# Optimization experiments

Hardware: AMD Instinct MI355X
Metric: run time of the kernel (lower is better)

Reference implementation:

```python
import jax, jax.numpy as jnp
import numpy as np

B, S, D, H = 2, 2048, 1024, 16
DK = D // H


def setup_inputs() -> dict:
    key = jax.random.key(0)
    ks = jax.random.split(key, 12)
    scale = 0.02
    inp = {
        "query": jax.random.normal(ks[0], (B, S, D), jnp.float32),
        "key_": jax.random.normal(ks[1], (B, S, D), jnp.float32),
        "value": jax.random.normal(ks[2], (B, S, D), jnp.float32),
        # causal mask; masked_fill where mask == 0
        "mask": jnp.tril(jnp.ones((S, S), jnp.int32))[None, None, :, :],
        # torch Linear weights are [out, in]; y = x @ W.T + b
        "Wq": jax.random.normal(ks[3], (D, D), jnp.float32) * scale,
        "bq": jax.random.normal(ks[4], (D,), jnp.float32) * scale,
        "Wk": jax.random.normal(ks[5], (D, D), jnp.float32) * scale,
        "bk": jax.random.normal(ks[6], (D,), jnp.float32) * scale,
        "Wv": jax.random.normal(ks[7], (D, D), jnp.float32) * scale,
        "bv": jax.random.normal(ks[8], (D,), jnp.float32) * scale,
        "Wo": jax.random.normal(ks[9], (D, D), jnp.float32) * scale,
        "bo": jax.random.normal(ks[10], (D,), jnp.float32) * scale,
    }
    return inp


def reference(query, key_, value, mask, Wq, bq, Wk, bk, Wv, bv, Wo, bo):
    # projections (torch Linear: x @ W.T + b)
    Q = query @ Wq.T + bq
    K = key_ @ Wk.T + bk
    V = value @ Wv.T + bv
    # [B, S, D] -> [B, H, S, DK]
    Q = Q.reshape(B, S, H, DK).transpose(0, 2, 1, 3)
    K = K.reshape(B, S, H, DK).transpose(0, 2, 1, 3)
    V = V.reshape(B, S, H, DK).transpose(0, 2, 1, 3)
    scores = jnp.einsum("bhqd,bhkd->bhqk", Q, K) / jnp.sqrt(jnp.float32(DK))
    scores = jnp.where(mask == 0, jnp.float32(-1e9), scores)
    attn = jax.nn.softmax(scores, axis=-1)
    # dropout is identity in eval mode
    context = jnp.einsum("bhqk,bhkd->bhqd", attn, V)
    context = context.transpose(0, 2, 1, 3).reshape(B, S, D)
    output = context @ Wo.T + bo
    return (output, attn)
```

## Files before the change

### kernel.cpp

```cpp
#include <hip/hip_runtime.h>
#include <hip/hip_bf16.h>

#define BB 2
#define SS 2048
#define DD 1024
#define HH 16

typedef __attribute__((ext_vector_type(8))) short bf16x8;
typedef __attribute__((ext_vector_type(4))) float f32x4;
typedef __attribute__((ext_vector_type(4))) unsigned int u32x4;
typedef __attribute__((ext_vector_type(2))) unsigned int u32x2;

__device__ inline unsigned short f2bf(float f) {
  unsigned int u = __float_as_uint(f);
  u += 0x7fff + ((u >> 16) & 1);
  return (unsigned short)(u >> 16);
}

__device__ inline void gll16(const void* g, void* l) {
  __builtin_amdgcn_global_load_lds(
      (const __attribute__((address_space(1))) unsigned int*)g,
      (__attribute__((address_space(3))) unsigned int*)l, 16, 0, 0);
}

__device__ inline int swz(int row, int col) {
  return row * 64 + ((((col >> 3) + row + (row >> 3)) & 7) << 3) + (col & 7);
}

__global__ void convert_all(const float* __restrict__ q, const float* __restrict__ k,
                            const float* __restrict__ v, const float* __restrict__ wq,
                            const float* __restrict__ wk, const float* __restrict__ wv,
                            const float* __restrict__ wo, unsigned short* __restrict__ dst) {
  int gi = blockIdx.x * 256 + threadIdx.x;
  long base = (long)gi * 4;
  if (base >= 16777216L) return;
  const float* src;
  long off;
  if (base < 12582912L) {
    int a = (int)(base >> 22);
    off = base & 4194303L;
    src = (a == 0) ? q : (a == 1 ? k : v);
  } else {
    long wb = base - 12582912L;
    int a = (int)(wb >> 20);
    off = wb & 1048575L;
    src = (a == 0) ? wq : (a == 1 ? wk : (a == 2 ? wv : wo));
  }
  const float4 f = *(const float4*)(src + off);
  ushort4 o;
  o.x = f2bf(f.x); o.y = f2bf(f.y); o.z = f2bf(f.z); o.w = f2bf(f.w);
  *(ushort4*)(dst + base) = o;
}

template <int OUT_F32>
__global__ __launch_bounds__(256, 3) void gemm_bt(const unsigned short* __restrict__ Aall,
                                                  const unsigned short* __restrict__ Wall,
                                                  const float* __restrict__ b0,
                                                  const float* __restrict__ b1,
                                                  const float* __restrict__ b2,
                                                  void* __restrict__ Call) {
  __shared__ unsigned short As[128 * 64];
  __shared__ unsigned short Bs[128 * 64];
  const int tid = threadIdx.x;
  const int lane = tid & 63;
  const int w = tid >> 6;
  const int wm = w >> 1, wn = w & 1;
  const int z = blockIdx.z;
  const int m0 = blockIdx.y * 128;
  const int n0 = blockIdx.x * 128;
  const unsigned short* A = Aall + (long)z * 4194304;
  const unsigned short* W = Wall + (long)z * 1048576;
  const float* bias = (z == 0) ? b0 : (z == 1 ? b1 : b2);
  const int r = lane & 15, g = lane >> 4;
  const int lrow = lane >> 3;
  const int lcol = (lane & 7) * 8;

  f32x4 acc[4][4];
#pragma unroll
  for (int i = 0; i < 4; i++)
#pragma unroll
    for (int j = 0; j < 4; j++) acc[i][j] = (f32x4){0.f, 0.f, 0.f, 0.f};

  for (int kt = 0; kt < 16; kt++) {
    const int k0 = kt * 64;
#pragma unroll
    for (int t = 0; t < 4; t++) {
      int row = w * 32 + t * 8 + lrow;
      gll16(A + (long)(m0 + row) * 1024 + k0 + lcol, &As[(w * 32 + t * 8) * 64]);
      gll16(W + (long)(n0 + row) * 1024 + k0 + lcol, &Bs[(w * 32 + t * 8) * 64]);
    }
    __syncthreads();
#pragma unroll
    for (int kk = 0; kk < 2; kk++) {
      bf16x8 af[4], bfr[4];
#pragma unroll
      for (int mi = 0; mi < 4; mi++)
        af[mi] = *(const bf16x8*)&As[(wm * 64 + mi * 16 + r) * 64 + kk * 32 + g * 8];
#pragma unroll
      for (int ni = 0; ni < 4; ni++)
        bfr[ni] = *(const bf16x8*)&Bs[(wn * 64 + ni * 16 + r) * 64 + kk * 32 + g * 8];
#pragma unroll
      for (int mi = 0; mi < 4; mi++)
#pragma unroll
        for (int ni = 0; ni < 4; ni++)
          acc[mi][ni] = __builtin_amdgcn_mfma_f32_16x16x32_bf16(af[mi], bfr[ni], acc[mi][ni], 0, 0, 0);
    }
    __syncthreads();
  }
#pragma unroll
  for (int ni = 0; ni < 4; ni++) {
    int n = n0 + wn * 64 + ni * 16 + r;
    float bv = bias[n];
#pragma unroll
    for (int mi = 0; mi < 4; mi++) {
      if (OUT_F32) {
#pragma unroll
        for (int reg = 0; reg < 4; reg++) {
          int m = m0 + wm * 64 + mi * 16 + g * 4 + reg;
          ((float*)Call)[(long)m * 1024 + n] = acc[mi][ni][reg] + bv;
        }
      } else if (z == 2) {
        int m = m0 + wm * 64 + mi * 16 + g * 4;
        ushort4 o;
        o.x = f2bf(acc[mi][ni][0] + bv);
        o.y = f2bf(acc[mi][ni][1] + bv);
        o.z = f2bf(acc[mi][ni][2] + bv);
        o.w = f2bf(acc[mi][ni][3] + bv);
        long idx = 2L * 4194304 + ((long)((m >> 11) * 1024 + n)) * 2048 + (m & 2047);
        *(ushort4*)((unsigned short*)Call + idx) = o;
      } else {
#pragma unroll
        for (int reg = 0; reg < 4; reg++) {
          int m = m0 + wm * 64 + mi * 16 + g * 4 + reg;
          ((unsigned short*)Call)[(long)z * 4194304 + (long)m * 1024 + n] =
              f2bf(acc[mi][ni][reg] + bv);
        }
      }
    }
  }
}

__global__ __launch_bounds__(256, 3) void attn_kernel(const unsigned short* __restrict__ Qb,
                                                      const unsigned short* __restrict__ Kb,
                                                      const unsigned short* __restrict__ Vtg,
                                                      unsigned short* __restrict__ Ctx,
                                                      float* __restrict__ attn) {
  __shared__ unsigned short Ks[2][64 * 64];
  __shared__ unsigned short Vs[2][64 * 64];
  __shared__ unsigned short Ps[64 * 64];
  const int tid = threadIdx.x;
  const int lane = tid & 63;
  const int w = tid >> 6;
  const int r = lane & 15, g = lane >> 4;
  const int h = blockIdx.y, b = blockIdx.z;
  const int bh = b * HH + h;
  const unsigned short* Kg = Kb + (long)b * SS * DD + h * 64;
  const unsigned short* Vg = Vtg + (long)bh * 64 * SS;
  float* attn_bh = attn + (long)bh * SS * SS;
  const int srow = tid >> 3;
  const int scg = tid & 7;

  for (int half = 0; half < 2; half++) {
    const int qt = half ? (31 - (int)blockIdx.x) : (int)blockIdx.x;
    const int q0 = qt * 64;
    const unsigned short* Qg = Qb + (long)(b * SS + q0) * DD + h * 64;
    bf16x8 aq0 = *(const bf16x8*)(Qg + (long)(16 * w + r) * DD + g * 8);
    bf16x8 aq1 = *(const bf16x8*)(Qg + (long)(16 * w + r) * DD + 32 + g * 8);

    u32x4 kpre[2];
#pragma unroll
    for (int it = 0; it < 2; it++)
      kpre[it] = *(const u32x4*)(Kg + (long)(it * 32 + srow) * DD + scg * 8);
    __syncthreads();
    float rs = 0.f;
    for (int kt = 0; kt <= qt; kt++) {
      unsigned short* kbuf = Ks[kt & 1];
#pragma unroll
      for (int it = 0; it < 2; it++)
        *(u32x4*)&kbuf[swz(it * 32 + srow, scg * 8)] = kpre[it];
      const int ktn = (kt < qt) ? kt + 1 : kt;
#pragma unroll
      for (int it = 0; it < 2; it++)
        kpre[it] = *(const u32x4*)(Kg + (long)(ktn * 64 + it * 32 + srow) * DD + scg * 8);
      __syncthreads();
#pragma unroll
      for (int mi = 0; mi < 4; mi++) {
        bf16x8 ak0 = *(const bf16x8*)&kbuf[swz(mi * 16 + r, g * 8)];
        bf16x8 ak1 = *(const bf16x8*)&kbuf[swz(mi * 16 + r, 32 + g * 8)];
        f32x4 sa = (f32x4){0.f, 0.f, 0.f, 0.f};
        sa = __builtin_amdgcn_mfma_f32_16x16x32_bf16(ak0, aq0, sa, 0, 0, 0);
        sa = __builtin_amdgcn_mfma_f32_16x16x32_bf16(ak1, aq1, sa, 0, 0, 0);
        if (kt == qt) {
#pragma unroll
          for (int reg = 0; reg < 4; reg++)
            rs += (mi * 16 + g * 4 + reg <= 16 * w + r) ? __expf(sa[reg] * 0.125f) : 0.f;
        } else {
#pragma unroll
          for (int reg = 0; reg < 4; reg++) rs += __expf(sa[reg] * 0.125f);
        }
      }
    }
    rs += __shfl_xor(rs, 16);
    rs += __shfl_xor(rs, 32);
    const float inv = 1.f / rs;

    f32x4 oacc[4];
#pragma unroll
    for (int dj = 0; dj < 4; dj++) oacc[dj] = (f32x4){0.f, 0.f, 0.f, 0.f};
    u32x4 vpre[2];
#pragma unroll
    for (int it = 0; it < 2; it++) {
      kpre[it] = *(const u32x4*)(Kg + (long)(it * 32 + srow) * DD + scg * 8);
      vpre[it] = *(const u32x4*)(Vg + (long)(it * 32 + srow) * SS + scg * 8);
    }
    __syncthreads();
    float* rowp = attn_bh + (long)(q0 + 16 * w + r) * SS;
    for (int kt = 0; kt <= qt; kt++) {
      unsigned short* kbuf = Ks[kt & 1];
      unsigned short* vbuf = Vs[kt & 1];
#pragma unroll
      for (int it = 0; it < 2; it++) {
        *(u32x4*)&kbuf[swz(it * 32 + srow, scg * 8)] = kpre[it];
        *(u32x4*)&vbuf[swz(it * 32 + srow, scg * 8)] = vpre[it];
      }
      const int ktn = (kt < qt) ? kt + 1 : kt;
#pragma unroll
      for (int it = 0; it < 2; it++) {
        kpre[it] = *(const u32x4*)(Kg + (long)(ktn * 64 + it * 32 + srow) * DD + scg * 8);
        vpre[it] = *(const u32x4*)(Vg + (long)(it * 32 + srow) * SS + ktn * 64 + scg * 8);
      }
      __syncthreads();
#pragma unroll
      for (int mi = 0; mi < 4; mi++) {
        bf16x8 ak0 = *(const bf16x8*)&kbuf[swz(mi * 16 + r, g * 8)];
        bf16x8 ak1 = *(const bf16x8*)&kbuf[swz(mi * 16 + r, 32 + g * 8)];
        f32x4 sa = (f32x4){0.f, 0.f, 0.f, 0.f};
        sa = __builtin_amdgcn_mfma_f32_16x16x32_bf16(ak0, aq0, sa, 0, 0, 0);
        sa = __builtin_amdgcn_mfma_f32_16x16x32_bf16(ak1, aq1, sa, 0, 0, 0);
        f32x4 p;
        if (kt == qt) {
#pragma unroll
          for (int reg = 0; reg < 4; reg++)
            p[reg] = (mi * 16 + g * 4 + reg <= 16 * w + r) ? __expf(sa[reg] * 0.125f) * inv : 0.f;
        } else {
#pragma unroll
          for (int reg = 0; reg < 4; reg++) p[reg] = __expf(sa[reg] * 0.125f) * inv;
        }
        *(f32x4*)(rowp + kt * 64 + mi * 16 + g * 4) = p;
        unsigned int p01 = (unsigned)f2bf(p[0]) | ((unsigned)f2bf(p[1]) << 16);
        unsigned int p23 = (unsigned)f2bf(p[2]) | ((unsigned)f2bf(p[3]) << 16);
        *(u32x2*)&Ps[swz(16 * w + r, mi * 16 + g * 4)] = (u32x2){p01, p23};
      }
#pragma unroll
      for (int kk = 0; kk < 2; kk++) {
        bf16x8 ap = *(const bf16x8*)&Ps[swz(16 * w + r, kk * 32 + g * 8)];
#pragma unroll
        for (int dj = 0; dj < 4; dj++) {
          bf16x8 bv = *(const bf16x8*)&vbuf[swz(dj * 16 + r, kk * 32 + g * 8)];
          oacc[dj] = __builtin_amdgcn_mfma_f32_16x16x32_bf16(ap, bv, oacc[dj], 0, 0, 0);
        }
      }
    }
#pragma unroll
    for (int dj = 0; dj < 4; dj++) {
#pragma unroll
      for (int reg = 0; reg < 4; reg++) {
        int rowg = q0 + 16 * w + g * 4 + reg;
        Ctx[(long)(b * SS + rowg) * DD + h * 64 + dj * 16 + r] = f2bf(oacc[dj][reg]);
      }
    }
    int zs = (qt + 1) * 64;
    if (zs < SS) {
      int zc = SS - zs;
      f32x4 zero = (f32x4){0.f, 0.f, 0.f, 0.f};
      for (int rr = 0; rr < 64; rr++) {
        float* rp = attn_bh + (long)(q0 + rr) * SS + zs;
        for (int cc = tid * 4; cc < zc; cc += 1024) *(f32x4*)(rp + cc) = zero;
      }
    }
  }
}

extern "C" void kernel_launch(void* const* d_in, const int* in_sizes, int n_in,
                              void* d_out, int out_size, void* d_ws, size_t ws_size,
                              hipStream_t stream) {
  const float* q  = (const float*)d_in[0];
  const float* k  = (const float*)d_in[1];
  const float* v  = (const float*)d_in[2];
  const float* wq = (const float*)d_in[4];
  const float* bq = (const float*)d_in[5];
  const float* wk = (const float*)d_in[6];
  const float* bk = (const float*)d_in[7];
  const float* wv = (const float*)d_in[8];
  const float* bv = (const float*)d_in[9];
  const float* wo = (const float*)d_in[10];
  const float* bo = (const float*)d_in[11];

  unsigned short* ws = (unsigned short*)d_ws;
  unsigned short* Xq  = ws;
  unsigned short* Wqb = ws + 12582912;
  unsigned short* Qb  = ws + 16777216;
  unsigned short* Ctx = ws + 29360128;
  float* outp = (float*)d_out;
  float* attn = outp + 4194304;

  convert_all<<<dim3(16384), dim3(256), 0, stream>>>(q, k, v, wq, wk, wv, wo, ws);
  gemm_bt<0><<<dim3(8, 32, 3), dim3(256), 0, stream>>>(Xq, Wqb, bq, bk, bv, (void*)Qb);
  attn_kernel<<<dim3(16, 16, 2), dim3(256), 0, stream>>>(Qb, Qb + 4194304, Qb + 8388608, Ctx, attn);
  gemm_bt<1><<<dim3(8, 32, 1), dim3(256), 0, stream>>>(Ctx, Wqb + 3145728, bo, bo, bo, (void*)outp);
}
```

Measured before the change: 738.3 us.

## Split attention KV tiles across two warp groups per block with cross-group reduction

```diff
diff --git a/kernel.cpp b/kernel.cpp
--- a/kernel.cpp
+++ b/kernel.cpp
@@ -140,69 +140,92 @@
   }
 }
 
-__global__ __launch_bounds__(256, 3) void attn_kernel(const unsigned short* __restrict__ Qb,
+__global__ __launch_bounds__(512, 4) void attn_kernel(const unsigned short* __restrict__ Qb,
                                                       const unsigned short* __restrict__ Kb,
                                                       const unsigned short* __restrict__ Vtg,
                                                       unsigned short* __restrict__ Ctx,
                                                       float* __restrict__ attn) {
-  __shared__ unsigned short Ks[2][64 * 64];
-  __shared__ unsigned short Vs[2][64 * 64];
-  __shared__ unsigned short Ps[64 * 64];
+  __shared__ unsigned short smem[40960];
+  unsigned short* KsA = smem;
+  unsigned short* KsB = smem + 8192;
+  unsigned short* VsA = smem + 16384;
+  unsigned short* VsB = smem + 24576;
+  unsigned short* PsG = smem + 32768;
+  float* rsbuf = (float*)(smem + 32768);
+  float* obuf = (float*)smem;
+
   const int tid = threadIdx.x;
   const int lane = tid & 63;
   const int w = tid >> 6;
+  const int grp = w >> 2;
+  const int wl = w & 3;
   const int r = lane & 15, g = lane >> 4;
+  const int gtid = tid & 255;
+  const int srow = gtid >> 3;
+  const int scg = gtid & 7;
+  unsigned short* Kbuf0 = grp ? KsB : KsA;
+  unsigned short* Vbuf0 = grp ? VsB : VsA;
+  unsigned short* Ps = PsG + grp * 4096;
+
   const int h = blockIdx.y, b = blockIdx.z;
   const int bh = b * HH + h;
   const unsigned short* Kg = Kb + (long)b * SS * DD + h * 64;
   const unsigned short* Vg = Vtg + (long)bh * 64 * SS;
   float* attn_bh = attn + (long)bh * SS * SS;
-  const int srow = tid >> 3;
-  const int scg = tid & 7;
 
   for (int half = 0; half < 2; half++) {
     const int qt = half ? (31 - (int)blockIdx.x) : (int)blockIdx.x;
     const int q0 = qt * 64;
     const unsigned short* Qg = Qb + (long)(b * SS + q0) * DD + h * 64;
-    bf16x8 aq0 = *(const bf16x8*)(Qg + (long)(16 * w + r) * DD + g * 8);
-    bf16x8 aq1 = *(const bf16x8*)(Qg + (long)(16 * w + r) * DD + 32 + g * 8);
+    const int R = (qt + 2) >> 1;
+
+    __syncthreads();
+    bf16x8 aq0 = *(const bf16x8*)(Qg + (long)(16 * wl + r) * DD + g * 8);
+    bf16x8 aq1 = *(const bf16x8*)(Qg + (long)(16 * wl + r) * DD + 32 + g * 8);
 
     u32x4 kpre[2];
 #pragma unroll
     for (int it = 0; it < 2; it++)
-      kpre[it] = *(const u32x4*)(Kg + (long)(it * 32 + srow) * DD + scg * 8);
-    __syncthreads();
+      kpre[it] = *(const u32x4*)(Kg + (long)(grp * 64 + it * 32 + srow) * DD + scg * 8);
     float rs = 0.f;
-    for (int kt = 0; kt <= qt; kt++) {
-      unsigned short* kbuf = Ks[kt & 1];
-#pragma unroll
-      for (int it = 0; it < 2; it++)
-        *(u32x4*)&kbuf[swz(it * 32 + srow, scg * 8)] = kpre[it];
-      const int ktn = (kt < qt) ? kt + 1 : kt;
+    for (int t = 0; t < R; t++) {
+      const int kt = 2 * t + grp;
+      unsigned short* kbuf = Kbuf0 + (t & 1) * 4096;
+      if (kt <= qt) {
+#pragma unroll
+        for (int it = 0; it < 2; it++)
+          *(u32x4*)&kbuf[swz(it * 32 + srow, scg * 8)] = kpre[it];
+      }
+      const int ktn = (kt + 2 <= qt) ? kt + 2 : 0;
 #pragma unroll
       for (int it = 0; it < 2; it++)
         kpre[it] = *(const u32x4*)(Kg + (long)(ktn * 64 + it * 32 + srow) * DD + scg * 8);
       __syncthreads();
-#pragma unroll
-      for (int mi = 0; mi < 4; mi++) {
-        bf16x8 ak0 = *(const bf16x8*)&kbuf[swz(mi * 16 + r, g * 8)];
-        bf16x8 ak1 = *(const bf16x8*)&kbuf[swz(mi * 16 + r, 32 + g * 8)];
-        f32x4 sa = (f32x4){0.f, 0.f, 0.f, 0.f};
-        sa = __builtin_amdgcn_mfma_f32_16x16x32_bf16(ak0, aq0, sa, 0, 0, 0);
-        sa = __builtin_amdgcn_mfma_f32_16x16x32_bf16(ak1, aq1, sa, 0, 0, 0);
-        if (kt == qt) {
-#pragma unroll
-          for (int reg = 0; reg < 4; reg++)
-            rs += (mi * 16 + g * 4 + reg <= 16 * w + r) ? __expf(sa[reg] * 0.125f) : 0.f;
-        } else {
-#pragma unroll
-          for (int reg = 0; reg < 4; reg++) rs += __expf(sa[reg] * 0.125f);
+      if (kt <= qt) {
+#pragma unroll
+        for (int mi = 0; mi < 4; mi++) {
+          bf16x8 ak0 = *(const bf16x8*)&kbuf[swz(mi * 16 + r, g * 8)];
+          bf16x8 ak1 = *(const bf16x8*)&kbuf[swz(mi * 16 + r, 32 + g * 8)];
+          f32x4 sa = (f32x4){0.f, 0.f, 0.f, 0.f};
+          sa = __builtin_amdgcn_mfma_f32_16x16x32_bf16(ak0, aq0, sa, 0, 0, 0);
+          sa = __builtin_amdgcn_mfma_f32_16x16x32_bf16(ak1, aq1, sa, 0, 0, 0);
+          if (kt == qt) {
+#pragma unroll
+            for (int reg = 0; reg < 4; reg++)
+              rs += (mi * 16 + g * 4 + reg <= 16 * wl + r) ? __expf(sa[reg] * 0.125f) : 0.f;
+          } else {
+#pragma unroll
+            for (int reg = 0; reg < 4; reg++) rs += __expf(sa[reg] * 0.125f);
+          }
         }
       }
     }
     rs += __shfl_xor(rs, 16);
     rs += __shfl_xor(rs, 32);
-    const float inv = 1.f / rs;
+    __syncthreads();
+    if (g == 0) rsbuf[grp * 64 + wl * 16 + r] = rs;
+    __syncthreads();
+    const float inv = 1.f / (rsbuf[wl * 16 + r] + rsbuf[64 + wl * 16 + r]);
 
     f32x4 oacc[4];
 #pragma unroll
@@ -210,63 +233,79 @@
     u32x4 vpre[2];
 #pragma unroll
     for (int it = 0; it < 2; it++) {
-      kpre[it] = *(const u32x4*)(Kg + (long)(it * 32 + srow) * DD + scg * 8);
-      vpre[it] = *(const u32x4*)(Vg + (long)(it * 32 + srow) * SS + scg * 8);
-    }
-    __syncthreads();
-    float* rowp = attn_bh + (long)(q0 + 16 * w + r) * SS;
-    for (int kt = 0; kt <= qt; kt++) {
-      unsigned short* kbuf = Ks[kt & 1];
-      unsigned short* vbuf = Vs[kt & 1];
-#pragma unroll
-      for (int it = 0; it < 2; it++) {
-        *(u32x4*)&kbuf[swz(it * 32 + srow, scg * 8)] = kpre[it];
-        *(u32x4*)&vbuf[swz(it * 32 + srow, scg * 8)] = vpre[it];
-      }
-      const int ktn = (kt < qt) ? kt + 1 : kt;
+      kpre[it] = *(const u32x4*)(Kg + (long)(grp * 64 + it * 32 + srow) * DD + scg * 8);
+      vpre[it] = *(const u32x4*)(Vg + (long)(it * 32 + srow) * SS + grp * 64 + scg * 8);
+    }
+    float* rowp = attn_bh + (long)(q0 + 16 * wl + r) * SS;
+    for (int t = 0; t < R; t++) {
+      const int kt = 2 * t + grp;
+      unsigned short* kbuf = Kbuf0 + (t & 1) * 4096;
+      unsigned short* vbuf = Vbuf0 + (t & 1) * 4096;
+      if (kt <= qt) {
+#pragma unroll
+        for (int it = 0; it < 2; it++) {
+          *(u32x4*)&kbuf[swz(it * 32 + srow, scg * 8)] = kpre[it];
+          *(u32x4*)&vbuf[swz(it * 32 + srow, scg * 8)] = vpre[it];
+        }
+      }
+      const int ktn = (kt + 2 <= qt) ? kt + 2 : 0;
 #pragma unroll
       for (int it = 0; it < 2; it++) {
         kpre[it] = *(const u32x4*)(Kg + (long)(ktn * 64 + it * 32 + srow) * DD + scg * 8);
         vpre[it] = *(const u32x4*)(Vg + (long)(it * 32 + srow) * SS + ktn * 64 + scg * 8);
       }
       __syncthreads();
-#pragma unroll
-      for (int mi = 0; mi < 4; mi++) {
-        bf16x8 ak0 = *(const bf16x8*)&kbuf[swz(mi * 16 + r, g * 8)];
-        bf16x8 ak1 = *(const bf16x8*)&kbuf[swz(mi * 16 + r, 32 + g * 8)];
-        f32x4 sa = (f32x4){0.f, 0.f, 0.f, 0.f};
-        sa = __builtin_amdgcn_mfma_f32_16x16x32_bf16(ak0, aq0, sa, 0, 0, 0);
-        sa = __builtin_amdgcn_mfma_f32_16x16x32_bf16(ak1, aq1, sa, 0, 0, 0);
-        f32x4 p;
-        if (kt == qt) {
-#pragma unroll
-          for (int reg = 0; reg < 4; reg++)
-            p[reg] = (mi * 16 + g * 4 + reg <= 16 * w + r) ? __expf(sa[reg] * 0.125f) * inv : 0.f;
-        } else {
-#pragma unroll
-          for (int reg = 0; reg < 4; reg++) p[reg] = __expf(sa[reg] * 0.125f) * inv;
-        }
-        *(f32x4*)(rowp + kt * 64 + mi * 16 + g * 4) = p;
-        unsigned int p01 = (unsigned)f2bf(p[0]) | ((unsigned)f2bf(p[1]) << 16);
-        unsigned int p23 = (unsigned)f2bf(p[2]) | ((unsigned)f2bf(p[3]) << 16);
-        *(u32x2*)&Ps[swz(16 * w + r, mi * 16 + g * 4)] = (u32x2){p01, p23};
-      }
-#pragma unroll
-      for (int kk = 0; kk < 2; kk++) {
-        bf16x8 ap = *(const bf16x8*)&Ps[swz(16 * w + r, kk * 32 + g * 8)];
-#pragma unroll
-        for (int dj = 0; dj < 4; dj++) {
-          bf16x8 bv = *(const bf16x8*)&vbuf[swz(dj * 16 + r, kk * 32 + g * 8)];
-          oacc[dj] = __builtin_amdgcn_mfma_f32_16x16x32_bf16(ap, bv, oacc[dj], 0, 0, 0);
-        }
-      }
-    }
-#pragma unroll
-    for (int dj = 0; dj < 4; dj++) {
-#pragma unroll
-      for (int reg = 0; reg < 4; reg++) {
-        int rowg = q0 + 16 * w + g * 4 + reg;
-        Ctx[(long)(b * SS + rowg) * DD + h * 64 + dj * 16 + r] = f2bf(oacc[dj][reg]);
+      if (kt <= qt) {
+#pragma unroll
+        for (int mi = 0; mi < 4; mi++) {
+          bf16x8 ak0 = *(const bf16x8*)&kbuf[swz(mi * 16 + r, g * 8)];
+          bf16x8 ak1 = *(const bf16x8*)&kbuf[swz(mi * 16 + r, 32 + g * 8)];
+          f32x4 sa = (f32x4){0.f, 0.f, 0.f, 0.f};
+          sa = __builtin_amdgcn_mfma_f32_16x16x32_bf16(ak0, aq0, sa, 0, 0, 0);
+          sa = __builtin_amdgcn_mfma_f32_16x16x32_bf16(ak1, aq1, sa, 0, 0, 0);
+          f32x4 p;
+          if (kt == qt) {
+#pragma unroll
+            for (int reg = 0; reg < 4; reg++)
+              p[reg] = (mi * 16 + g * 4 + reg <= 16 * wl + r) ? __expf(sa[reg] * 0.125f) * inv : 0.f;
+          } else {
+#pragma unroll
+            for (int reg = 0; reg < 4; reg++) p[reg] = __expf(sa[reg] * 0.125f) * inv;
+          }
+          __builtin_nontemporal_store(p, (f32x4*)(rowp + kt * 64 + mi * 16 + g * 4));
+          unsigned int p01 = (unsigned)f2bf(p[0]) | ((unsigned)f2bf(p[1]) << 16);
+          unsigned int p23 = (unsigned)f2bf(p[2]) | ((unsigned)f2bf(p[3]) << 16);
+          *(u32x2*)&Ps[swz(16 * wl + r, mi * 16 + g * 4)] = (u32x2){p01, p23};
+        }
+#pragma unroll
+        for (int kk = 0; kk < 2; kk++) {
+          bf16x8 ap = *(const bf16x8*)&Ps[swz(16 * wl + r, kk * 32 + g * 8)];
+#pragma unroll
+          for (int dj = 0; dj < 4; dj++) {
+            bf16x8 bv = *(const bf16x8*)&vbuf[swz(dj * 16 + r, kk * 32 + g * 8)];
+            oacc[dj] = __builtin_amdgcn_mfma_f32_16x16x32_bf16(ap, bv, oacc[dj], 0, 0, 0);
+          }
+        }
+      }
+    }
+    __syncthreads();
+    if (grp == 1) {
+#pragma unroll
+      for (int dj = 0; dj < 4; dj++)
+#pragma unroll
+        for (int reg = 0; reg < 4; reg++)
+          obuf[(wl * 16 + g * 4 + reg) * 64 + dj * 16 + r] = oacc[dj][reg];
+    }
+    __syncthreads();
+    if (grp == 0) {
+#pragma unroll
+      for (int dj = 0; dj < 4; dj++) {
+#pragma unroll
+        for (int reg = 0; reg < 4; reg++) {
+          int rowl = wl * 16 + g * 4 + reg;
+          float val = oacc[dj][reg] + obuf[rowl * 64 + dj * 16 + r];
+          Ctx[(long)(b * SS + q0 + rowl) * DD + h * 64 + dj * 16 + r] = f2bf(val);
+        }
       }
     }
     int zs = (qt + 1) * 64;
@@ -275,7 +314,8 @@
       f32x4 zero = (f32x4){0.f, 0.f, 0.f, 0.f};
       for (int rr = 0; rr < 64; rr++) {
         float* rp = attn_bh + (long)(q0 + rr) * SS + zs;
-        for (int cc = tid * 4; cc < zc; cc += 1024) *(f32x4*)(rp + cc) = zero;
+        for (int cc = tid * 4; cc < zc; cc += 2048)
+          __builtin_nontemporal_store(zero, (f32x4*)(rp + cc));
       }
     }
   }
@@ -306,6 +346,6 @@
 
   convert_all<<<dim3(16384), dim3(256), 0, stream>>>(q, k, v, wq, wk, wv, wo, ws);
   gemm_bt<0><<<dim3(8, 32, 3), dim3(256), 0, stream>>>(Xq, Wqb, bq, bk, bv, (void*)Qb);
-  attn_kernel<<<dim3(16, 16, 2), dim3(256), 0, stream>>>(Qb, Qb + 4194304, Qb + 8388608, Ctx, attn);
+  attn_kernel<<<dim3(16, 16, 2), dim3(512), 0, stream>>>(Qb, Qb + 4194304, Qb + 8388608, Ctx, attn);
   gemm_bt<1><<<dim3(8, 32, 1), dim3(256), 0, stream>>>(Ctx, Wqb + 3145728, bo, bo, bo, (void*)outp);
 }
```

After: 751.8 us. Within noise of the previous version (+1.8%).
